# Kernel optimization log

Hardware: AMD Instinct MI355X
Metric: run time of the kernel (lower is better)

The kernel has to match this reference:

```python
import jax, jax.numpy as jnp
import numpy as np

B, S, D, H = 4, 4096, 2048, 16
DH = D // H
SCALE = float(np.sqrt(DH))


def setup_inputs() -> dict:
    key = jax.random.key(0)
    ks = jax.random.split(key, 11)
    std = 1.0 / np.sqrt(D)
    inp = {
        "query": jax.random.normal(ks[0], (B, S, D), jnp.float32),
        "key": jax.random.normal(ks[1], (B, S, D), jnp.float32),
        "value": jax.random.normal(ks[2], (B, S, D), jnp.float32),
        "Wq": jax.random.normal(ks[3], (D, D), jnp.float32) * std,
        "bq": jax.random.normal(ks[4], (D,), jnp.float32) * std,
        "Wk": jax.random.normal(ks[5], (D, D), jnp.float32) * std,
        "bk": jax.random.normal(ks[6], (D,), jnp.float32) * std,
        "Wv": jax.random.normal(ks[7], (D, D), jnp.float32) * std,
        "bv": jax.random.normal(ks[8], (D,), jnp.float32) * std,
        "Wo": jax.random.normal(ks[9], (D, D), jnp.float32) * std,
        "bo": jax.random.normal(ks[10], (D,), jnp.float32) * std,
    }
    return inp


def reference(query, key, value, Wq, bq, Wk, bk, Wv, bv, Wo, bo):
    # Linear projections (torch nn.Linear: x @ W^T + b)
    Q = query @ Wq.T + bq          # [B,S,D]
    K = key @ Wk.T + bk
    V = value @ Wv.T + bv
    Q = Q.reshape(B, S, H, DH)
    K = K.reshape(B, S, H, DH)
    V = V.reshape(B, S, H, DH)
    # NOTE: original torch code does NOT transpose heads to dim 1, so the
    # matmul contracts over head-dim pairs at each position: scores [B,S,H,H]
    scores = jnp.einsum('bsid,bsjd->bsij', Q, K) / SCALE
    attention = jax.nn.softmax(scores, axis=-1)   # softmax over heads (faithful)
    x = jnp.einsum('bsij,bsjd->bsid', attention, V)  # [B,S,H,DH]
    # permute(0,2,1,3) -> [B,H,S,DH], then view(B,-1,D) -> [B,S,D]
    x = jnp.transpose(x, (0, 2, 1, 3)).reshape(B, S, D)
    out = x @ Wo.T + bo
    return out, attention
```

## Files before the change

kernel.cpp:

```cpp
#include <hip/hip_runtime.h>


#define DEV __device__ __forceinline__

using short8  = __attribute__((ext_vector_type(8))) short;
using ushort8 = __attribute__((ext_vector_type(8))) unsigned short;
using f32x4   = __attribute__((ext_vector_type(4))) float;
using u16x8   = __attribute__((ext_vector_type(8))) unsigned short;

constexpr int BATCH = 4, SEQ = 4096, DIM = 2048;
constexpr int GM = BATCH * SEQ;
constexpr int GN = DIM, GK = DIM;

DEV unsigned short f2bf(float f) {
  unsigned int u = __builtin_bit_cast(unsigned int, f);
  u += 0x7FFFu + ((u >> 16) & 1u);
  return (unsigned short)(u >> 16);
}
DEV float bf2f(unsigned short h) {
  unsigned int u = ((unsigned int)h) << 16;
  return __builtin_bit_cast(float, u);
}

DEV void gload16(const void* g, void* l) {
  __builtin_amdgcn_global_load_lds(
      (const __attribute__((address_space(1))) void*)g,
      (__attribute__((address_space(3))) void*)l, 16, 0, 0);
}

#define BAR    __builtin_amdgcn_s_barrier()
#define LGKM0  asm volatile("s_waitcnt lgkmcnt(0)" ::: "memory")
#define LGKM8  asm volatile("s_waitcnt lgkmcnt(8)" ::: "memory")
#define VMC(N) asm volatile("s_waitcnt vmcnt(" #N ")" ::: "memory")
#define SCHED0 __builtin_amdgcn_sched_barrier(0)
#define PRIO1  __builtin_amdgcn_s_setprio(1)
#define PRIO0  __builtin_amdgcn_s_setprio(0)
#define MFMA16(a, b, c) __builtin_amdgcn_mfma_f32_16x16x32_bf16(a, b, c, 0, 0, 0)

__global__ void cvt_f32_bf16(const float* __restrict__ src,
                             unsigned short* __restrict__ dst, int n) {
  int i = (blockIdx.x * blockDim.x + threadIdx.x) * 4;
  if (i >= n) return;
  f32x4 f = *(const f32x4*)(src + i);
  ushort4 o;
  o.x = f2bf(f[0]); o.y = f2bf(f[1]); o.z = f2bf(f[2]); o.w = f2bf(f[3]);
  *(ushort4*)(dst + i) = o;
}

template <bool OUTF32>
__global__ __launch_bounds__(512, 2)
void gemm256(const unsigned short* __restrict__ Ap,
             const unsigned short* __restrict__ Bp,
             const float* __restrict__ bias, void* __restrict__ Cp) {
  constexpr int BK = 64, KT = GK / BK;
  __shared__ unsigned short As[2][2][128 * 64];
  __shared__ unsigned short Bs[2][2][128 * 64];

  const int tid  = threadIdx.x;
  const int lane = tid & 63;
  const int wv   = tid >> 6;
  const int wm   = wv >> 2, wn = wv & 3;

  int bid = (int)blockIdx.x;
  const int xcd = bid & 7, rr = bid >> 3;
  const int gg = rr >> 5, jj = rr & 31;
  const int mt = xcd * 8 + gg * 4 + (jj & 3);
  const int nt = jj >> 2;
  const int bm0 = mt * 256, bn0 = nt * 256;

  int dst_[2];
  size_t offA_[2][2], offB_[2][2];
#pragma unroll
  for (int r = 0; r < 2; ++r) {
    int d = tid * 16 + r * 8192;
    int s = d ^ (((d >> 7) & 7) << 4);
    int row = s >> 7, col = (s & 127) >> 1;
    dst_[r] = d;
#pragma unroll
    for (int h = 0; h < 2; ++h) {
      offA_[h][r] = (size_t)(bm0 + h * 128 + row) * GK + col;
      offB_[h][r] = (size_t)(bn0 + h * 128 + row) * GK + col;
    }
  }

  const int r16 = lane & 15, kb = (lane >> 4) * 16;
  const int bhalf = wn >> 1;
  const int brow0 = (wn & 1) * 64 + r16;

  f32x4 acc[8][4] = {};
  short8 af[4][2], bl[2][2], bh[2][2];

  auto stA = [&](int buf, int h, int T) {
#pragma unroll
    for (int r = 0; r < 2; ++r)
      gload16(Ap + offA_[h][r] + (size_t)T * BK, (char*)&As[buf][h][0] + dst_[r]);
  };
  auto stB = [&](int buf, int h, int T) {
#pragma unroll
    for (int r = 0; r < 2; ++r)
      gload16(Bp + offB_[h][r] + (size_t)T * BK, (char*)&Bs[buf][h][0] + dst_[r]);
  };
  auto ldf = [&](const unsigned short* base, int rowh, int ks) -> short8 {
    int a = (rowh * 128 + ks * 64 + kb) ^ ((rowh & 7) << 4);
    return *(const short8*)((const char*)base + a);
  };

  stA(0, 0, 0); stA(0, 1, 0);
  stB(0, 0, 0); stB(0, 1, 0);
  stB(1, 0, 1); stB(1, 1, 1);
  VMC(4);
  BAR;

  for (int T = 0; T < KT; ++T) {
    const int bb = T & 1;
    const unsigned short* Abase = &As[bb][wm][0];
    const unsigned short* Bbase = &Bs[bb][bhalf][0];
    const bool m1 = (T + 1 < KT), m2 = (T + 2 < KT);

#pragma unroll
    for (int m = 0; m < 4; ++m) {
      af[m][0] = ldf(Abase, m * 16 + r16, 0);
      af[m][1] = ldf(Abase, m * 16 + r16, 1);
    }
#pragma unroll
    for (int n = 0; n < 2; ++n) {
      bl[n][0] = ldf(Bbase, brow0 + n * 16, 0);
      bl[n][1] = ldf(Bbase, brow0 + n * 16, 1);
    }
    if (m1) stA(bb ^ 1, 0, T + 1);
    LGKM8; SCHED0; BAR; LGKM0; SCHED0;
    PRIO1;
#pragma unroll
    for (int m = 0; m < 4; ++m)
#pragma unroll
      for (int n = 0; n < 2; ++n) {
        acc[m][n] = MFMA16(af[m][0], bl[n][0], acc[m][n]);
        acc[m][n] = MFMA16(af[m][1], bl[n][1], acc[m][n]);
      }
    PRIO0; SCHED0; BAR;

#pragma unroll
    for (int n = 0; n < 2; ++n) {
      bh[n][0] = ldf(Bbase, brow0 + 32 + n * 16, 0);
      bh[n][1] = ldf(Bbase, brow0 + 32 + n * 16, 1);
    }
    if (m1) stA(bb ^ 1, 1, T + 1);
    SCHED0; BAR; LGKM0; SCHED0;
    PRIO1;
#pragma unroll
    for (int m = 0; m < 4; ++m)
#pragma unroll
      for (int n = 0; n < 2; ++n) {
        acc[m][2 + n] = MFMA16(af[m][0], bh[n][0], acc[m][2 + n]);
        acc[m][2 + n] = MFMA16(af[m][1], bh[n][1], acc[m][2 + n]);
      }
    PRIO0; SCHED0; BAR;

#pragma unroll
    for (int m = 0; m < 4; ++m) {
      af[m][0] = ldf(Abase, 64 + m * 16 + r16, 0);
      af[m][1] = ldf(Abase, 64 + m * 16 + r16, 1);
    }
    if (m2) stB(bb, 0, T + 2);
    SCHED0; BAR; LGKM0; SCHED0;
    PRIO1;
#pragma unroll
    for (int m = 0; m < 4; ++m)
#pragma unroll
      for (int n = 0; n < 2; ++n) {
        acc[4 + m][2 + n] = MFMA16(af[m][0], bh[n][0], acc[4 + m][2 + n]);
        acc[4 + m][2 + n] = MFMA16(af[m][1], bh[n][1], acc[4 + m][2 + n]);
      }
    PRIO0; SCHED0; BAR;

    if (m2) {
      stB(bb, 1, T + 2);
      SCHED0; VMC(4);
    } else {
      SCHED0; VMC(0);
    }
    SCHED0; BAR;
    PRIO1;
#pragma unroll
    for (int m = 0; m < 4; ++m)
#pragma unroll
      for (int n = 0; n < 2; ++n) {
        acc[4 + m][n] = MFMA16(af[m][0], bl[n][0], acc[4 + m][n]);
        acc[4 + m][n] = MFMA16(af[m][1], bl[n][1], acc[4 + m][n]);
      }
    PRIO0; SCHED0; BAR;
  }

  float bs[4];
#pragma unroll
  for (int n = 0; n < 4; ++n) bs[n] = bias[bn0 + wn * 64 + n * 16 + r16];
  const int rb = (lane >> 4) * 4;
#pragma unroll
  for (int m = 0; m < 8; ++m)
#pragma unroll
    for (int i = 0; i < 4; ++i) {
      const size_t row = (size_t)bm0 + wm * 128 + m * 16 + rb + i;
#pragma unroll
      for (int n = 0; n < 4; ++n) {
        const int col = bn0 + wn * 64 + n * 16 + r16;
        float v = acc[m][n][i] + bs[n];
        if constexpr (OUTF32)
          ((float*)Cp)[row * GN + col] = v;
        else
          ((unsigned short*)Cp)[row * GN + col] = f2bf(v);
      }
    }
}

__global__ __launch_bounds__(256)
void attn_kernel(const unsigned short* __restrict__ Qb,
                 const unsigned short* __restrict__ Kb,
                 const unsigned short* __restrict__ Vb,
                 float* __restrict__ attnOut,
                 unsigned short* __restrict__ X2) {
  __shared__ float qf[16 * 128];
  __shared__ float kf[16 * 132];
  __shared__ float vf[16 * 128];
  __shared__ float sc[256];

  const int t = threadIdx.x;
  const int p = blockIdx.x;
  const size_t rowoff = (size_t)p * DIM;

  {
    const int e = t * 8;
    u16x8 qv = *(const u16x8*)(Qb + rowoff + e);
    u16x8 kv = *(const u16x8*)(Kb + rowoff + e);
    u16x8 vv = *(const u16x8*)(Vb + rowoff + e);
    const int r = t >> 4, c = (t & 15) * 8;
#pragma unroll
    for (int j = 0; j < 8; ++j) qf[r * 128 + c + j] = bf2f(qv[j]);
#pragma unroll
    for (int j = 0; j < 8; ++j) kf[r * 132 + c + j] = bf2f(kv[j]);
#pragma unroll
    for (int j = 0; j < 8; ++j) vf[r * 128 + c + j] = bf2f(vv[j]);
  }
  __syncthreads();

  const int i = t >> 4, j = t & 15;
  float s = 0.f;
#pragma unroll
  for (int d4 = 0; d4 < 32; ++d4) {
    f32x4 q4 = *(const f32x4*)&qf[i * 128 + d4 * 4];
    f32x4 k4 = *(const f32x4*)&kf[j * 132 + d4 * 4];
    s = fmaf(q4[0], k4[0], fmaf(q4[1], k4[1], fmaf(q4[2], k4[2], fmaf(q4[3], k4[3], s))));
  }
  s *= 0.08838834764831845f;

  float mx = s;
#pragma unroll
  for (int off = 8; off; off >>= 1) mx = fmaxf(mx, __shfl_xor(mx, off, 16));
  float ex = __expf(s - mx);
  float sum = ex;
#pragma unroll
  for (int off = 8; off; off >>= 1) sum += __shfl_xor(sum, off, 16);
  float a = ex / sum;

  attnOut[(size_t)p * 256 + t] = a;
  sc[t] = a;
  __syncthreads();

  const int dh0 = j * 8;
  float o[8] = {};
#pragma unroll
  for (int jjq = 0; jjq < 16; ++jjq) {
    float aij = sc[i * 16 + jjq];
#pragma unroll
    for (int e2 = 0; e2 < 8; ++e2)
      o[e2] = fmaf(aij, vf[jjq * 128 + dh0 + e2], o[e2]);
  }
  const int b = p >> 12, spos = p & 4095;
  const int row = i * 256 + (spos >> 4);
  const int col = ((spos & 15) << 7) + dh0;
  ushort8 pk;
#pragma unroll
  for (int e2 = 0; e2 < 8; ++e2) pk[e2] = f2bf(o[e2]);
  *(ushort8*)(X2 + (size_t)b * (SEQ * DIM) + (size_t)row * DIM + col) = pk;
}

extern "C" void kernel_launch(void* const* d_in, const int* in_sizes, int n_in,
                              void* d_out, int out_size, void* d_ws,
                              size_t ws_size, hipStream_t stream) {
  const float* q  = (const float*)d_in[0];
  const float* k  = (const float*)d_in[1];
  const float* v  = (const float*)d_in[2];
  const float* Wq = (const float*)d_in[3];
  const float* bq = (const float*)d_in[4];
  const float* Wk = (const float*)d_in[5];
  const float* bk = (const float*)d_in[6];
  const float* Wv = (const float*)d_in[7];
  const float* bv = (const float*)d_in[8];
  const float* Wo = (const float*)d_in[9];
  const float* bo = (const float*)d_in[10];

  const size_t NE = (size_t)GM * GK;
  const size_t WE = (size_t)GK * GN;

  unsigned short* ws16 = (unsigned short*)d_ws;
  unsigned short* Wq_b = ws16;
  unsigned short* Wk_b = Wq_b + WE;
  unsigned short* Wv_b = Wk_b + WE;
  unsigned short* Wo_b = Wv_b + WE;
  unsigned short* Qb   = Wo_b + WE;
  unsigned short* Kb   = Qb + NE;
  unsigned short* Vb   = Kb + NE;
  unsigned short* X2   = Vb + NE;
  unsigned short* Qin  = X2 + NE;
  unsigned short* Kin  = Qin + NE;
  unsigned short* Vin  = Kin + NE;

  float* outMain = (float*)d_out;
  float* attnOut = outMain + (size_t)GM * GN;

  cvt_f32_bf16<<<WE / 1024, 256, 0, stream>>>(Wq, Wq_b, (int)WE);
  cvt_f32_bf16<<<WE / 1024, 256, 0, stream>>>(Wk, Wk_b, (int)WE);
  cvt_f32_bf16<<<WE / 1024, 256, 0, stream>>>(Wv, Wv_b, (int)WE);
  cvt_f32_bf16<<<WE / 1024, 256, 0, stream>>>(Wo, Wo_b, (int)WE);

  cvt_f32_bf16<<<NE / 1024, 256, 0, stream>>>(q, Qin, (int)NE);
  cvt_f32_bf16<<<NE / 1024, 256, 0, stream>>>(k, Kin, (int)NE);
  cvt_f32_bf16<<<NE / 1024, 256, 0, stream>>>(v, Vin, (int)NE);

  constexpr int G256 = (GM / 256) * (GN / 256);

  gemm256<false><<<G256, 512, 0, stream>>>(Qin, Wq_b, bq, Qb);
  gemm256<false><<<G256, 512, 0, stream>>>(Kin, Wk_b, bk, Kb);
  gemm256<false><<<G256, 512, 0, stream>>>(Vin, Wv_b, bv, Vb);

  attn_kernel<<<GM, 256, 0, stream>>>(Qb, Kb, Vb, attnOut, X2);

  gemm256<true><<<G256, 512, 0, stream>>>(X2, Wo_b, bo, outMain);
}
```

Measured before the change: 857.4 us.

## Use 4-wave 256x256 GEMM with 128x128 per-wave tiles and fuse conversions

The GEMM moves from 8 waves of 128x64 each to 4 waves of 128x128 each, with a reworked double-buffered LDS pipeline. Fragments for the next K-step are prefetched while MFMAs run, and there are fewer barriers per iteration. The aim is more MFMA work per LDS read and less synchronisation, at the cost of higher register pressure (64 accumulators per thread) and one block per CU. The seven separate f32-to-bf16 conversion launches are merged into a single kernel that writes 8 elements per thread.

Result: slower. 950.7 us (+10.9%).

```diff
diff --git a/kernel.cpp b/kernel.cpp
--- a/kernel.cpp
+++ b/kernel.cpp
@@ -30,36 +30,69 @@
 
 #define BAR    __builtin_amdgcn_s_barrier()
 #define LGKM0  asm volatile("s_waitcnt lgkmcnt(0)" ::: "memory")
-#define LGKM8  asm volatile("s_waitcnt lgkmcnt(8)" ::: "memory")
+#define LGKM(N) asm volatile("s_waitcnt lgkmcnt(" #N ")" ::: "memory")
 #define VMC(N) asm volatile("s_waitcnt vmcnt(" #N ")" ::: "memory")
 #define SCHED0 __builtin_amdgcn_sched_barrier(0)
 #define PRIO1  __builtin_amdgcn_s_setprio(1)
 #define PRIO0  __builtin_amdgcn_s_setprio(0)
 #define MFMA16(a, b, c) __builtin_amdgcn_mfma_f32_16x16x32_bf16(a, b, c, 0, 0, 0)
 
-__global__ void cvt_f32_bf16(const float* __restrict__ src,
-                             unsigned short* __restrict__ dst, int n) {
-  int i = (blockIdx.x * blockDim.x + threadIdx.x) * 4;
-  if (i >= n) return;
-  f32x4 f = *(const f32x4*)(src + i);
-  ushort4 o;
-  o.x = f2bf(f[0]); o.y = f2bf(f[1]); o.z = f2bf(f[2]); o.w = f2bf(f[3]);
-  *(ushort4*)(dst + i) = o;
+#define QUAD(AF, BF, MO, NO)                                          \
+  _Pragma("unroll") for (int m_ = 0; m_ < 4; ++m_)                    \
+  _Pragma("unroll") for (int n_ = 0; n_ < 4; ++n_) {                  \
+    acc[(MO) + m_][(NO) + n_] =                                       \
+        MFMA16(AF[m_][0], BF[n_][0], acc[(MO) + m_][(NO) + n_]);      \
+    acc[(MO) + m_][(NO) + n_] =                                       \
+        MFMA16(AF[m_][1], BF[n_][1], acc[(MO) + m_][(NO) + n_]);      \
+  }
+
+constexpr size_t NE_C = (size_t)GM * GK;
+constexpr size_t WE_C = (size_t)GK * GN;
+
+__global__ __launch_bounds__(256)
+void cvt_all(const float* __restrict__ q, const float* __restrict__ k,
+             const float* __restrict__ v, const float* __restrict__ Wq,
+             const float* __restrict__ Wk, const float* __restrict__ Wv,
+             const float* __restrict__ Wo,
+             unsigned short* __restrict__ Qin, unsigned short* __restrict__ Kin,
+             unsigned short* __restrict__ Vin, unsigned short* __restrict__ Wqb,
+             unsigned short* __restrict__ Wkb, unsigned short* __restrict__ Wvb,
+             unsigned short* __restrict__ Wob) {
+  size_t gi = ((size_t)blockIdx.x * 256 + threadIdx.x) * 8;
+  const float* src;
+  unsigned short* dst;
+  size_t off;
+  if (gi < NE_C)            { src = q;  dst = Qin; off = gi; }
+  else if (gi < 2 * NE_C)   { src = k;  dst = Kin; off = gi - NE_C; }
+  else if (gi < 3 * NE_C)   { src = v;  dst = Vin; off = gi - 2 * NE_C; }
+  else {
+    size_t w = gi - 3 * NE_C;
+    if (w < WE_C)           { src = Wq; dst = Wqb; off = w; }
+    else if (w < 2 * WE_C)  { src = Wk; dst = Wkb; off = w - WE_C; }
+    else if (w < 3 * WE_C)  { src = Wv; dst = Wvb; off = w - 2 * WE_C; }
+    else                    { src = Wo; dst = Wob; off = w - 3 * WE_C; }
+  }
+  f32x4 f0 = *(const f32x4*)(src + off);
+  f32x4 f1 = *(const f32x4*)(src + off + 4);
+  ushort8 o;
+#pragma unroll
+  for (int j = 0; j < 4; ++j) { o[j] = f2bf(f0[j]); o[4 + j] = f2bf(f1[j]); }
+  *(ushort8*)(dst + off) = o;
 }
 
 template <bool OUTF32>
-__global__ __launch_bounds__(512, 2)
-void gemm256(const unsigned short* __restrict__ Ap,
-             const unsigned short* __restrict__ Bp,
-             const float* __restrict__ bias, void* __restrict__ Cp) {
+__global__ __launch_bounds__(256, 1)
+void gemm256p(const unsigned short* __restrict__ Ap,
+              const unsigned short* __restrict__ Bp,
+              const float* __restrict__ bias, void* __restrict__ Cp) {
   constexpr int BK = 64, KT = GK / BK;
-  __shared__ unsigned short As[2][2][128 * 64];
-  __shared__ unsigned short Bs[2][2][128 * 64];
+  __shared__ unsigned short As[2][256 * BK];
+  __shared__ unsigned short Bs[2][256 * BK];
 
   const int tid  = threadIdx.x;
   const int lane = tid & 63;
   const int wv   = tid >> 6;
-  const int wm   = wv >> 2, wn = wv & 3;
+  const int wm   = wv >> 1, wn = wv & 1;
 
   int bid = (int)blockIdx.x;
   const int xcd = bid & 7, rr = bid >> 3;
@@ -68,132 +101,88 @@
   const int nt = jj >> 2;
   const int bm0 = mt * 256, bn0 = nt * 256;
 
-  int dst_[2];
-  size_t offA_[2][2], offB_[2][2];
-#pragma unroll
-  for (int r = 0; r < 2; ++r) {
-    int d = tid * 16 + r * 8192;
+  int offA[8];
+#pragma unroll
+  for (int r = 0; r < 8; ++r) {
+    int d = tid * 16 + r * 4096;
     int s = d ^ (((d >> 7) & 7) << 4);
     int row = s >> 7, col = (s & 127) >> 1;
-    dst_[r] = d;
-#pragma unroll
-    for (int h = 0; h < 2; ++h) {
-      offA_[h][r] = (size_t)(bm0 + h * 128 + row) * GK + col;
-      offB_[h][r] = (size_t)(bn0 + h * 128 + row) * GK + col;
-    }
-  }
+    offA[r] = (bm0 + row) * GK + col;
+  }
+  const int dAB = (bn0 - bm0) * GK;
 
   const int r16 = lane & 15, kb = (lane >> 4) * 16;
-  const int bhalf = wn >> 1;
-  const int brow0 = (wn & 1) * 64 + r16;
-
-  f32x4 acc[8][4] = {};
-  short8 af[4][2], bl[2][2], bh[2][2];
-
-  auto stA = [&](int buf, int h, int T) {
-#pragma unroll
-    for (int r = 0; r < 2; ++r)
-      gload16(Ap + offA_[h][r] + (size_t)T * BK, (char*)&As[buf][h][0] + dst_[r]);
+
+  f32x4 acc[8][8] = {};
+  short8 al[4][2], ah[4][2], bl[4][2], bh[4][2];
+
+  auto stA = [&](int buf, int T) {
+#pragma unroll
+    for (int r = 0; r < 8; ++r)
+      gload16(Ap + (size_t)offA[r] + (size_t)T * BK,
+              (char*)&As[buf][0] + (tid * 16 + r * 4096));
   };
-  auto stB = [&](int buf, int h, int T) {
-#pragma unroll
-    for (int r = 0; r < 2; ++r)
-      gload16(Bp + offB_[h][r] + (size_t)T * BK, (char*)&Bs[buf][h][0] + dst_[r]);
+  auto stB = [&](int buf, int T) {
+#pragma unroll
+    for (int r = 0; r < 8; ++r)
+      gload16(Bp + (size_t)(offA[r] + dAB) + (size_t)T * BK,
+              (char*)&Bs[buf][0] + (tid * 16 + r * 4096));
   };
-  auto ldf = [&](const unsigned short* base, int rowh, int ks) -> short8 {
-    int a = (rowh * 128 + ks * 64 + kb) ^ ((rowh & 7) << 4);
+  auto ldf = [&](const unsigned short* base, int row, int ks) -> short8 {
+    int a = (row * 128 + ks * 64 + kb) ^ ((row & 7) << 4);
     return *(const short8*)((const char*)base + a);
   };
-
-  stA(0, 0, 0); stA(0, 1, 0);
-  stB(0, 0, 0); stB(0, 1, 0);
-  stB(1, 0, 1); stB(1, 1, 1);
-  VMC(4);
-  BAR;
+  auto rdS = [&](short8 (&dst)[4][2], const unsigned short* base, int row0) {
+#pragma unroll
+    for (int m = 0; m < 4; ++m) {
+      dst[m][0] = ldf(base, row0 + m * 16 + r16, 0);
+      dst[m][1] = ldf(base, row0 + m * 16 + r16, 1);
+    }
+  };
+
+  stA(0, 0); stB(0, 0);
+  VMC(0); SCHED0; BAR;
+  stA(1, 1); stB(1, 1);
+  rdS(al, &As[0][0], wm * 128);
+  rdS(bl, &Bs[0][0], wn * 128);
 
   for (int T = 0; T < KT; ++T) {
     const int bb = T & 1;
-    const unsigned short* Abase = &As[bb][wm][0];
-    const unsigned short* Bbase = &Bs[bb][bhalf][0];
+    const unsigned short* Ac = &As[bb][0];
+    const unsigned short* Bc = &Bs[bb][0];
+    const unsigned short* An = &As[bb ^ 1][0];
+    const unsigned short* Bn = &Bs[bb ^ 1][0];
     const bool m1 = (T + 1 < KT), m2 = (T + 2 < KT);
 
-#pragma unroll
-    for (int m = 0; m < 4; ++m) {
-      af[m][0] = ldf(Abase, m * 16 + r16, 0);
-      af[m][1] = ldf(Abase, m * 16 + r16, 1);
+    rdS(bh, Bc, wn * 128 + 64);
+    LGKM(8); SCHED0;
+    PRIO1; QUAD(al, bl, 0, 0); PRIO0;
+
+    rdS(ah, Ac, wm * 128 + 64);
+    LGKM(8); SCHED0;
+    PRIO1; QUAD(al, bh, 0, 4); PRIO0;
+
+    LGKM0; SCHED0;
+    if (m1) {
+      if (m2) { VMC(8); } else { VMC(0); }
+      SCHED0; BAR;
+      if (m2) stA(bb, T + 2);
+      rdS(al, An, wm * 128);
     }
-#pragma unroll
-    for (int n = 0; n < 2; ++n) {
-      bl[n][0] = ldf(Bbase, brow0 + n * 16, 0);
-      bl[n][1] = ldf(Bbase, brow0 + n * 16, 1);
+    PRIO1; QUAD(ah, bh, 4, 4); PRIO0;
+
+    if (m1) {
+      if (m2) { VMC(8); } else { VMC(0); }
+      SCHED0; BAR;
+      if (m2) stB(bb, T + 2);
     }
-    if (m1) stA(bb ^ 1, 0, T + 1);
-    LGKM8; SCHED0; BAR; LGKM0; SCHED0;
-    PRIO1;
-#pragma unroll
-    for (int m = 0; m < 4; ++m)
-#pragma unroll
-      for (int n = 0; n < 2; ++n) {
-        acc[m][n] = MFMA16(af[m][0], bl[n][0], acc[m][n]);
-        acc[m][n] = MFMA16(af[m][1], bl[n][1], acc[m][n]);
-      }
-    PRIO0; SCHED0; BAR;
-
-#pragma unroll
-    for (int n = 0; n < 2; ++n) {
-      bh[n][0] = ldf(Bbase, brow0 + 32 + n * 16, 0);
-      bh[n][1] = ldf(Bbase, brow0 + 32 + n * 16, 1);
-    }
-    if (m1) stA(bb ^ 1, 1, T + 1);
-    SCHED0; BAR; LGKM0; SCHED0;
-    PRIO1;
-#pragma unroll
-    for (int m = 0; m < 4; ++m)
-#pragma unroll
-      for (int n = 0; n < 2; ++n) {
-        acc[m][2 + n] = MFMA16(af[m][0], bh[n][0], acc[m][2 + n]);
-        acc[m][2 + n] = MFMA16(af[m][1], bh[n][1], acc[m][2 + n]);
-      }
-    PRIO0; SCHED0; BAR;
-
-#pragma unroll
-    for (int m = 0; m < 4; ++m) {
-      af[m][0] = ldf(Abase, 64 + m * 16 + r16, 0);
-      af[m][1] = ldf(Abase, 64 + m * 16 + r16, 1);
-    }
-    if (m2) stB(bb, 0, T + 2);
-    SCHED0; BAR; LGKM0; SCHED0;
-    PRIO1;
-#pragma unroll
-    for (int m = 0; m < 4; ++m)
-#pragma unroll
-      for (int n = 0; n < 2; ++n) {
-        acc[4 + m][2 + n] = MFMA16(af[m][0], bh[n][0], acc[4 + m][2 + n]);
-        acc[4 + m][2 + n] = MFMA16(af[m][1], bh[n][1], acc[4 + m][2 + n]);
-      }
-    PRIO0; SCHED0; BAR;
-
-    if (m2) {
-      stB(bb, 1, T + 2);
-      SCHED0; VMC(4);
-    } else {
-      SCHED0; VMC(0);
-    }
-    SCHED0; BAR;
-    PRIO1;
-#pragma unroll
-    for (int m = 0; m < 4; ++m)
-#pragma unroll
-      for (int n = 0; n < 2; ++n) {
-        acc[4 + m][n] = MFMA16(af[m][0], bl[n][0], acc[4 + m][n]);
-        acc[4 + m][n] = MFMA16(af[m][1], bl[n][1], acc[4 + m][n]);
-      }
-    PRIO0; SCHED0; BAR;
-  }
-
-  float bs[4];
-#pragma unroll
-  for (int n = 0; n < 4; ++n) bs[n] = bias[bn0 + wn * 64 + n * 16 + r16];
+    PRIO1; QUAD(ah, bl, 4, 0); PRIO0;
+    if (m1) rdS(bl, Bn, wn * 128);
+  }
+
+  float bs[8];
+#pragma unroll
+  for (int n = 0; n < 8; ++n) bs[n] = bias[bn0 + wn * 128 + n * 16 + r16];
   const int rb = (lane >> 4) * 4;
 #pragma unroll
   for (int m = 0; m < 8; ++m)
@@ -201,8 +190,8 @@
     for (int i = 0; i < 4; ++i) {
       const size_t row = (size_t)bm0 + wm * 128 + m * 16 + rb + i;
 #pragma unroll
-      for (int n = 0; n < 4; ++n) {
-        const int col = bn0 + wn * 64 + n * 16 + r16;
+      for (int n = 0; n < 8; ++n) {
+        const int col = bn0 + wn * 128 + n * 16 + r16;
         float v = acc[m][n][i] + bs[n];
         if constexpr (OUTF32)
           ((float*)Cp)[row * GN + col] = v;
@@ -298,8 +287,8 @@
   const float* Wo = (const float*)d_in[9];
   const float* bo = (const float*)d_in[10];
 
-  const size_t NE = (size_t)GM * GK;
-  const size_t WE = (size_t)GK * GN;
+  const size_t NE = NE_C;
+  const size_t WE = WE_C;
 
   unsigned short* ws16 = (unsigned short*)d_ws;
   unsigned short* Wq_b = ws16;
@@ -317,22 +306,17 @@
   float* outMain = (float*)d_out;
   float* attnOut = outMain + (size_t)GM * GN;
 
-  cvt_f32_bf16<<<WE / 1024, 256, 0, stream>>>(Wq, Wq_b, (int)WE);
-  cvt_f32_bf16<<<WE / 1024, 256, 0, stream>>>(Wk, Wk_b, (int)WE);
-  cvt_f32_bf16<<<WE / 1024, 256, 0, stream>>>(Wv, Wv_b, (int)WE);
-  cvt_f32_bf16<<<WE / 1024, 256, 0, stream>>>(Wo, Wo_b, (int)WE);
-
-  cvt_f32_bf16<<<NE / 1024, 256, 0, stream>>>(q, Qin, (int)NE);
-  cvt_f32_bf16<<<NE / 1024, 256, 0, stream>>>(k, Kin, (int)NE);
-  cvt_f32_bf16<<<NE / 1024, 256, 0, stream>>>(v, Vin, (int)NE);
+  const int cvt_blocks = (int)((3 * NE + 4 * WE) / 8 / 256);
+  cvt_all<<<cvt_blocks, 256, 0, stream>>>(q, k, v, Wq, Wk, Wv, Wo,
+                                          Qin, Kin, Vin, Wq_b, Wk_b, Wv_b, Wo_b);
 
   constexpr int G256 = (GM / 256) * (GN / 256);
 
-  gemm256<false><<<G256, 512, 0, stream>>>(Qin, Wq_b, bq, Qb);
-  gemm256<false><<<G256, 512, 0, stream>>>(Kin, Wk_b, bk, Kb);
-  gemm256<false><<<G256, 512, 0, stream>>>(Vin, Wv_b, bv, Vb);
+  gemm256p<false><<<G256, 256, 0, stream>>>(Qin, Wq_b, bq, Qb);
+  gemm256p<false><<<G256, 256, 0, stream>>>(Kin, Wk_b, bk, Kb);
+  gemm256p<false><<<G256, 256, 0, stream>>>(Vin, Wv_b, bv, Vb);
 
   attn_kernel<<<GM, 256, 0, stream>>>(Qb, Kb, Vb, attnOut, X2);
 
-  gemm256<true><<<G256, 512, 0, stream>>>(X2, Wo_b, bo, outMain);
-}
+  gemm256p<true><<<G256, 256, 0, stream>>>(X2, Wo_b, bo, outMain);
+}
```
